# Performance work log

Hardware: AMD Instinct MI355X
Metric: run time of the kernel (lower is better)

## Reference

```python
import jax, jax.numpy as jnp
import numpy as np

NEG_INF = -1e9
START_IDX = 1

def lstm_step(h, c, x_t, Wih, Whh, b):
    g = x_t @ Wih.T + h @ Whh.T + b
    i, f, gg, o = jnp.split(g, 4, axis=-1)  # torch gate order i,f,g,o
    c_new = jax.nn.sigmoid(f) * c + jax.nn.sigmoid(i) * jnp.tanh(gg)
    h_new = jax.nn.sigmoid(o) * jnp.tanh(c_new)
    return h_new, c_new

def masked_lstm(x, valid, Wih, Whh, b):
    # x: [B,S,E], valid: [B,S] bool. Emulates packed-sequence semantics:
    # state frozen and outputs zeroed past each sequence's length.
    B = x.shape[0]; H = Whh.shape[1]
    def step(carry, inp):
        h, c = carry
        x_t, v = inp
        hn, cn = lstm_step(h, c, x_t, Wih, Whh, b)
        v = v[:, None]
        h = jnp.where(v, hn, h); c = jnp.where(v, cn, c)
        return (h, c), jnp.where(v, hn, jnp.zeros_like(hn))
    z = jnp.zeros((B, H), x.dtype)
    (h, c), outs = jax.lax.scan(step, (z, z), (x.transpose(1, 0, 2), valid.T))
    return outs.transpose(1, 0, 2), h, c

def bilstm_encoder(x, lens, Wih_f, Whh_f, b_f, Wih_b, Whh_b, b_b):
    B, S, _ = x.shape
    pos = jnp.arange(S)[None, :]
    valid = pos < lens[:, None]
    out_f, h_f, c_f = masked_lstm(x, valid, Wih_f, Whh_f, b_f)
    # reverse each sequence within its valid length for the backward direction
    rev = jnp.clip(lens[:, None] - 1 - pos, 0, S - 1)  # [B,S]
    x_rev = jnp.take_along_axis(x, rev[:, :, None], axis=1)
    out_r, h_b, c_b = masked_lstm(x_rev, valid, Wih_b, Whh_b, b_b)
    out_b = jnp.take_along_axis(out_r, rev[:, :, None], axis=1) * valid[:, :, None]
    enc = jnp.concatenate([out_f, out_b], -1)          # [B,S,ENC_HID]
    h = jnp.concatenate([h_f, h_b], -1)                # [B,ENC_HID]
    c = jnp.concatenate([c_f, c_b], -1)
    return enc, h, c


def setup_inputs() -> dict:
    key = jax.random.key(0)
    ks = jax.random.split(key, 24)
    B, S, T = 32, 64, 64
    V_SRC, V_TGT, P, E, H2, HD = 50265, 32000, 768, 512, 256, 512
    n = lambda k, sh, s=0.05: (s * jax.random.normal(k, sh)).astype(jnp.float32)
    inp = {
        'xs': jax.random.randint(ks[0], (B, S), 0, V_SRC),
        'x_lens': jax.random.randint(ks[1], (B,), 32, S + 1).astype(jnp.int32),
        'ys': jax.random.randint(ks[2], (B, T + 1), 0, V_TGT),
        'src_emb': n(ks[3], (V_SRC, P)),
        'W_tr': n(ks[4], (E, P)), 'b_tr': jnp.zeros((E,), jnp.float32),
        'Wih_f': n(ks[5], (4 * H2, E)), 'Whh_f': n(ks[6], (4 * H2, H2)), 'b_f': jnp.zeros((4 * H2,), jnp.float32),
        'Wih_b': n(ks[7], (4 * H2, E)), 'Whh_b': n(ks[8], (4 * H2, H2)), 'b_b': jnp.zeros((4 * H2,), jnp.float32),
        'W_attn': n(ks[9], (HD, 2 * HD + HD)), 'b_attn': jnp.zeros((HD,), jnp.float32),
        'v_attn': (jax.random.normal(ks[10], (HD,)) / np.sqrt(HD)).astype(jnp.float32),
        'tgt_emb': n(ks[11], (V_TGT, E)),
        'W_comb': n(ks[12], (HD, E + HD)), 'b_comb': jnp.zeros((HD,), jnp.float32),
        'Wih_d': n(ks[13], (4 * HD, E)), 'Whh_d': n(ks[14], (4 * HD, HD)), 'b_d': jnp.zeros((4 * HD,), jnp.float32),
        'W_out': n(ks[15], (V_TGT, HD)), 'b_out': jnp.zeros((V_TGT,), jnp.float32),
    }
    return inp


def reference(xs, x_lens, ys, src_emb, W_tr, b_tr, Wih_f, Whh_f, b_f,
              Wih_b, Whh_b, b_b, W_attn, b_attn, v_attn, tgt_emb,
              W_comb, b_comb, Wih_d, Whh_d, b_d, W_out, b_out):
    # source embedding (pretrained adapter stub = lookup) + transform
    x = src_emb[xs] @ W_tr.T + b_tr                     # [B,S,E]
    enc, h, c = bilstm_encoder(x, x_lens, Wih_f, Whh_f, b_f, Wih_b, Whh_b, b_b)
    B, S = xs.shape
    T = ys.shape[1] - 1
    HD = Whh_d.shape[1]
    # split attention linear into hidden part and encoder part (precompute latter)
    W_h, W_e = W_attn[:, :2 * HD], W_attn[:, 2 * HD:]
    enc_proj = enc @ W_e.T                              # [B,S,HD]
    src_mask = jnp.arange(S)[None, :] < x_lens[:, None]
    # teacher forcing with ratio 1.0: inputs are [START, ys[:,1:T]]
    tokens = jnp.concatenate([jnp.full((B, 1), START_IDX, ys.dtype), ys[:, 1:T]], axis=1)

    def step(carry, tok):
        h, c = carry
        emb = tgt_emb[tok]                              # [B,E]
        hid = jnp.concatenate([h, c], -1)               # [B,2*HD]
        energy = jnp.tanh(enc_proj + (hid @ W_h.T + b_attn)[:, None, :])
        scores = jnp.where(src_mask, energy @ v_attn, NEG_INF)
        attn = jax.nn.softmax(scores, axis=1)           # [B,S]
        ctx = jnp.einsum('bs,bse->be', attn, enc)
        xi = jax.nn.relu(jnp.concatenate([emb, ctx], -1) @ W_comb.T + b_comb)
        h, c = lstm_step(h, c, xi, Wih_d, Whh_d, b_d)
        out = jax.nn.log_softmax(h @ W_out.T + b_out, axis=-1)
        return (h, c), out

    _, outs = jax.lax.scan(step, (h, c), tokens.T)      # outs: [T,B,V]
    return outs.transpose(1, 0, 2)                      # [B,T,V]
```

## Files before the change

kernel.cpp:

```cpp
#include <hip/hip_runtime.h>
#include <math.h>

#define B_  32
#define S_  64
#define T_  64
#define P_  768
#define E_  512
#define H2_ 256
#define G2_ 1024
#define HD_ 512
#define V_  32000
#define NWG 256

__device__ __forceinline__ float sigf(float x) {
    return 1.0f / (1.0f + __expf(-x));
}
__device__ __forceinline__ float tanh_fast(float x) {
    return 1.0f - 2.0f / (__expf(2.0f * x) + 1.0f);
}

__global__ void k_prep(const int* __restrict__ ys,
                       const float* __restrict__ Whh_f, const float* __restrict__ Whh_b,
                       float* __restrict__ WhhT_f, float* __restrict__ WhhT_b,
                       int* __restrict__ tokens, unsigned* __restrict__ bar)
{
    int i = blockIdx.x * blockDim.x + threadIdx.x;
    int n = gridDim.x * blockDim.x;
    for (int idx = i; idx < G2_ * H2_; idx += n) {
        int k = idx / G2_, g = idx % G2_;
        WhhT_f[idx] = Whh_f[g * H2_ + k];
        WhhT_b[idx] = Whh_b[g * H2_ + k];
    }
    for (int idx = i; idx < T_ * B_; idx += n) {
        int t = idx / B_, b = idx % B_;
        tokens[idx] = (t == 0) ? 1 : ys[b * (T_ + 1) + t];
    }
    for (int idx = i; idx < 160; idx += n) bar[idx] = 0u;
}

__global__ __launch_bounds__(256)
void gemm_f32(const float* __restrict__ A, const int* __restrict__ gidx, int lda,
              const float* __restrict__ W, int ldw, int woff,
              const float* __restrict__ bias,
              float* __restrict__ C, int ldc, int K)
{
    __shared__ __align__(16) float As[16][64];
    __shared__ __align__(16) float Bs[16][64];
    const int m0 = blockIdx.y * 64;
    const int n0 = blockIdx.x * 64;
    const int tid = threadIdx.x;
    const int tm = tid & 15, tn = tid >> 4;
    const int la_m = tid >> 2;
    const int la_k = (tid & 3) * 4;
    float acc[4][4] = {};

    const int am = m0 + la_m;
    const float* arow = A + (long)(gidx ? gidx[am] : am) * lda;
    const float* wrow = W + (long)(n0 + la_m) * ldw + woff;

    for (int k0 = 0; k0 < K; k0 += 16) {
        float4 av = *(const float4*)(arow + k0 + la_k);
        float4 wv = *(const float4*)(wrow + k0 + la_k);
        As[la_k + 0][la_m] = av.x; As[la_k + 1][la_m] = av.y;
        As[la_k + 2][la_m] = av.z; As[la_k + 3][la_m] = av.w;
        Bs[la_k + 0][la_m] = wv.x; Bs[la_k + 1][la_m] = wv.y;
        Bs[la_k + 2][la_m] = wv.z; Bs[la_k + 3][la_m] = wv.w;
        __syncthreads();
        #pragma unroll
        for (int kk = 0; kk < 16; kk++) {
            float4 a = *(const float4*)&As[kk][tm * 4];
            float4 b = *(const float4*)&Bs[kk][tn * 4];
            acc[0][0] += a.x * b.x; acc[0][1] += a.x * b.y; acc[0][2] += a.x * b.z; acc[0][3] += a.x * b.w;
            acc[1][0] += a.y * b.x; acc[1][1] += a.y * b.y; acc[1][2] += a.y * b.z; acc[1][3] += a.y * b.w;
            acc[2][0] += a.z * b.x; acc[2][1] += a.z * b.y; acc[2][2] += a.z * b.z; acc[2][3] += a.z * b.w;
            acc[3][0] += a.w * b.x; acc[3][1] += a.w * b.y; acc[3][2] += a.w * b.z; acc[3][3] += a.w * b.w;
        }
        __syncthreads();
    }
    float b0 = bias ? bias[n0 + tn * 4 + 0] : 0.f;
    float b1 = bias ? bias[n0 + tn * 4 + 1] : 0.f;
    float b2 = bias ? bias[n0 + tn * 4 + 2] : 0.f;
    float b3 = bias ? bias[n0 + tn * 4 + 3] : 0.f;
    #pragma unroll
    for (int i = 0; i < 4; i++) {
        long m = m0 + tm * 4 + i;
        float4 o = make_float4(acc[i][0] + b0, acc[i][1] + b1, acc[i][2] + b2, acc[i][3] + b3);
        *(float4*)&C[m * ldc + n0 + tn * 4] = o;
    }
}

__global__ __launch_bounds__(1024)
void k_encoder(const float* __restrict__ gpre_f, const float* __restrict__ gpre_b,
               const float* __restrict__ WhhT_f, const float* __restrict__ WhhT_b,
               const int* __restrict__ x_lens,
               float* __restrict__ enc, float* __restrict__ hid, float* __restrict__ xh0)
{
    const int b   = blockIdx.x >> 1;
    const int dir = blockIdx.x & 1;
    const float* gpre = dir ? gpre_b : gpre_f;
    const float* WT   = dir ? WhhT_b : WhhT_f;
    const int len = x_lens[b];
    __shared__ float h_lds[H2_];
    __shared__ float g_lds[G2_];
    const int tid = threadIdx.x;
    float c = 0.f;
    if (tid < H2_) h_lds[tid] = 0.f;
    __syncthreads();

    for (int t = 0; t < S_; t++) {
        bool valid = t < len;
        if (valid) {
            int s_in = dir ? (len - 1 - t) : t;
            float acc = gpre[(long)(b * S_ + s_in) * G2_ + tid];
            #pragma unroll 8
            for (int k = 0; k < H2_; k++)
                acc += h_lds[k] * WT[k * G2_ + tid];
            g_lds[tid] = acc;
            __syncthreads();
            if (tid < H2_) {
                float gi = g_lds[tid], gf = g_lds[H2_ + tid];
                float gg = g_lds[2 * H2_ + tid], go = g_lds[3 * H2_ + tid];
                c = sigf(gf) * c + sigf(gi) * tanh_fast(gg);
                float hn = sigf(go) * tanh_fast(c);
                h_lds[tid] = hn;
                enc[(long)(b * S_ + s_in) * E_ + dir * H2_ + tid] = hn;
            }
            __syncthreads();
        } else {
            if (tid < H2_)
                enc[(long)(b * S_ + t) * E_ + dir * H2_ + tid] = 0.f;
        }
    }
    if (tid < H2_) {
        hid[b * 1024 + dir * H2_ + tid]       = h_lds[tid];
        hid[b * 1024 + 512 + dir * H2_ + tid] = c;
        xh0[b * 1024 + 512 + dir * H2_ + tid] = h_lds[tid];
    }
}

__device__ __forceinline__ void grid_bar(unsigned* bar, int w, int tid)
{
    __syncthreads();
    if (tid == 0) {
        __threadfence();
        unsigned a = __hip_atomic_fetch_add(&bar[16 * (w & 7)], 1u,
                        __ATOMIC_RELAXED, __HIP_MEMORY_SCOPE_AGENT);
        unsigned target = (a >> 5) + 1u;
        if ((a & 31u) == 31u) {
            unsigned m = __hip_atomic_fetch_add(&bar[128], 1u,
                            __ATOMIC_RELAXED, __HIP_MEMORY_SCOPE_AGENT);
            if ((m & 7u) == 7u)
                __hip_atomic_store(&bar[144], (m >> 3) + 1u,
                                   __ATOMIC_RELAXED, __HIP_MEMORY_SCOPE_AGENT);
        }
        while (__hip_atomic_load(&bar[144], __ATOMIC_RELAXED,
                                 __HIP_MEMORY_SCOPE_AGENT) < target)
            __builtin_amdgcn_s_sleep(8);
        __threadfence();
    }
    __syncthreads();
}

__global__ __launch_bounds__(256, 1)
void k_decoder(const float* __restrict__ enc, const float* __restrict__ encp,
               const float* __restrict__ embW,
               const float* __restrict__ W_attn, const float* __restrict__ b_attn,
               const float* __restrict__ v_attn, const float* __restrict__ W_comb,
               const float* __restrict__ Wih_d, const float* __restrict__ Whh_d,
               const float* __restrict__ b_d,
               const int* __restrict__ x_lens,
               float* __restrict__ hid, float* __restrict__ xh0,
               float* __restrict__ xh1, float* __restrict__ attq,
               float* __restrict__ ctxg, float* __restrict__ Hall,
               unsigned* __restrict__ bar)
{
    const int w = blockIdx.x;
    const int tid = threadIdx.x;

    __shared__ float WdL[8 * 1028];
    __shared__ float WhL[4 * 1032];
    __shared__ float WcL[4 * 520];
    __shared__ float red[256];
    __shared__ float bsc[832];
    __shared__ float g_l[8 * 33];

    for (int i = tid; i < 8 * 1024; i += 256) {
        int lr = i >> 10, k = i & 1023;
        int row = 512 * (lr & 3) + 2 * w + (lr >> 2);
        WdL[lr * 1028 + k] = (k < 512) ? Wih_d[row * 512 + k]
                                       : Whh_d[row * 512 + (k - 512)];
    }
    for (int i = tid; i < 4 * 1024; i += 256) {
        int lr = i >> 10, k = i & 1023;
        WhL[lr * 1032 + k] = W_attn[(long)(4 * (w >> 1) + lr) * 1536 + k];
    }
    for (int i = tid; i < 4 * 512; i += 256) {
        int lr = i >> 9, k = i & 511;
        WcL[lr * 520 + k] = W_comb[(long)(4 * (w >> 1) + lr) * 1024 + 512 + k];
    }
    __syncthreads();

    const int o  = tid >> 2;
    const int ks = tid & 3;
    const int bl = o >> 2, lr = o & 3;
    const int ab = 16 * (w & 1) + bl;
    const int an = 4 * (w >> 1) + lr;
    const int r8 = tid & 7, b8 = tid >> 3;

    for (int t = 0; t < T_; t++) {
        float* xh_cur  = (t & 1) ? xh1 : xh0;
        float* xh_next = (t & 1) ? xh0 : xh1;

        {
            const float* hr = hid + ab * 1024;
            const float* wr = WhL + lr * 1032;
            float acc = 0.f;
            #pragma unroll 8
            for (int i = 0; i < 64; i++) {
                int k = 16 * i + 4 * ks;
                float4 a = *(const float4*)(hr + k);
                float4 v = *(const float4*)(wr + k);
                acc += a.x * v.x + a.y * v.y + a.z * v.z + a.w * v.w;
            }
            red[tid] = acc;
            __syncthreads();
            if (tid < 64) {
                int b2 = 16 * (w & 1) + (tid >> 2);
                int n2 = 4 * (w >> 1) + (tid & 3);
                float s = red[tid * 4] + red[tid * 4 + 1]
                        + red[tid * 4 + 2] + red[tid * 4 + 3];
                attq[b2 * 512 + n2] = s + b_attn[n2];
            }
        }
        grid_bar(bar, w, tid);

        if (w < 32) {
            float* aq   = bsc;
            float* part = bsc + 512;
            float* p    = bsc + 768;
            aq[tid]       = attq[w * 512 + tid];
            aq[tid + 256] = attq[w * 512 + 256 + tid];
            __syncthreads();
            {
                int s = tid >> 2, q = tid & 3;
                const float* ep = encp + (long)(w * S_ + s) * 512;
                float acc = 0.f;
                #pragma unroll 4
                for (int i = 0; i < 128; i++) {
                    int e = q + 4 * i;
                    acc += v_attn[e] * tanh_fast(ep[e] + aq[e]);
                }
                part[s * 4 + q] = acc;
            }
            __syncthreads();
            if (tid < 64) {
                float sc = part[tid * 4] + part[tid * 4 + 1]
                         + part[tid * 4 + 2] + part[tid * 4 + 3];
                if (tid >= x_lens[w]) sc = -1e9f;
                float m = sc;
                for (int off = 32; off; off >>= 1) m = fmaxf(m, __shfl_xor(m, off));
                float e = __expf(sc - m);
                float sum = e;
                for (int off = 32; off; off >>= 1) sum += __shfl_xor(sum, off);
                p[tid] = e / sum;
            }
            __syncthreads();
            float c0 = 0.f, c1 = 0.f;
            for (int s2 = 0; s2 < S_; s2++) {
                float pp = p[s2];
                const float* er = enc + (long)(w * S_ + s2) * 512;
                c0 += pp * er[tid];
                c1 += pp * er[tid + 256];
            }
            ctxg[w * 512 + tid]       = c0;
            ctxg[w * 512 + 256 + tid] = c1;
        }
        grid_bar(bar, w, tid);

        {
            const float* cr = ctxg + ab * 512;
            const float* wr = WcL + lr * 520;
            float acc = 0.f;
            #pragma unroll 8
            for (int i = 0; i < 32; i++) {
                int k = 16 * i + 4 * ks;
                float4 a = *(const float4*)(cr + k);
                float4 v = *(const float4*)(wr + k);
                acc += a.x * v.x + a.y * v.y + a.z * v.z + a.w * v.w;
            }
            red[tid] = acc;
            __syncthreads();
            if (tid < 64) {
                int b2 = 16 * (w & 1) + (tid >> 2);
                int n2 = 4 * (w >> 1) + (tid & 3);
                float s = red[tid * 4] + red[tid * 4 + 1]
                        + red[tid * 4 + 2] + red[tid * 4 + 3];
                float val = s + embW[((long)t * 32 + b2) * 512 + n2];
                xh_cur[b2 * 1024 + n2] = fmaxf(val, 0.f);
            }
        }
        grid_bar(bar, w, tid);

        {
            const float* ar = xh_cur + b8 * 1024;
            const float* wl = WdL + r8 * 1028;
            float acc = 0.f;
            #pragma unroll 8
            for (int q = 0; q < 256; q++) {
                float4 a = *(const float4*)(ar + 4 * q);
                float4 v = *(const float4*)(wl + 4 * q);
                acc += a.x * v.x + a.y * v.y + a.z * v.z + a.w * v.w;
            }
            int row = 512 * (r8 & 3) + 2 * w + (r8 >> 2);
            g_l[r8 * 33 + b8] = acc + b_d[row];
            __syncthreads();
            if (tid < 64) {
                int bb = tid & 31, hl = tid >> 5;
                int hu = 2 * w + hl;
                float gi = g_l[(hl * 4 + 0) * 33 + bb];
                float gf = g_l[(hl * 4 + 1) * 33 + bb];
                float gg = g_l[(hl * 4 + 2) * 33 + bb];
                float go = g_l[(hl * 4 + 3) * 33 + bb];
                float c_old = hid[bb * 1024 + 512 + hu];
                float c_new = sigf(gf) * c_old + sigf(gi) * tanh_fast(gg);
                float h_new = sigf(go) * tanh_fast(c_new);
                hid[bb * 1024 + hu] = h_new;
                hid[bb * 1024 + 512 + hu] = c_new;
                xh_next[bb * 1024 + 512 + hu] = h_new;
                Hall[((long)bb * T_ + t) * 512 + hu] = h_new;
            }
        }
        grid_bar(bar, w, tid);
    }
}

__global__ __launch_bounds__(256)
void k_lse(const float* __restrict__ Cl, float* __restrict__ lse)
{
    const int r = blockIdx.x;
    const float* row = Cl + (long)r * V_;
    const int tid = threadIdx.x;
    __shared__ float red[4];
    float m = -1e30f;
    for (int i = tid; i < V_; i += 256) m = fmaxf(m, row[i]);
    for (int off = 32; off; off >>= 1) m = fmaxf(m, __shfl_xor(m, off));
    int w = tid >> 6;
    if ((tid & 63) == 0) red[w] = m;
    __syncthreads();
    m = fmaxf(fmaxf(red[0], red[1]), fmaxf(red[2], red[3]));
    __syncthreads();
    float s = 0.f;
    for (int i = tid; i < V_; i += 256) s += __expf(row[i] - m);
    for (int off = 32; off; off >>= 1) s += __shfl_xor(s, off);
    if ((tid & 63) == 0) red[w] = s;
    __syncthreads();
    if (tid == 0) {
        s = red[0] + red[1] + red[2] + red[3];
        lse[r] = m + __logf(s);
    }
}

__global__ void k_logsub(float* __restrict__ C, const float* __restrict__ lse)
{
    long n4 = (long)2048 * V_ / 4;
    long stride = (long)gridDim.x * blockDim.x;
    for (long i = (long)blockIdx.x * blockDim.x + threadIdx.x; i < n4; i += stride) {
        float4 v = ((float4*)C)[i];
        float l = lse[(i * 4) / V_];
        v.x -= l; v.y -= l; v.z -= l; v.w -= l;
        ((float4*)C)[i] = v;
    }
}

extern "C" void kernel_launch(void* const* d_in, const int* in_sizes, int n_in,
                              void* d_out, int out_size, void* d_ws, size_t ws_size,
                              hipStream_t stream)
{
    const int*   xs     = (const int*)  d_in[0];
    const int*   x_lens = (const int*)  d_in[1];
    const int*   ys     = (const int*)  d_in[2];
    const float* src_emb= (const float*)d_in[3];
    const float* W_tr   = (const float*)d_in[4];
    const float* b_tr   = (const float*)d_in[5];
    const float* Wih_f  = (const float*)d_in[6];
    const float* Whh_f  = (const float*)d_in[7];
    const float* b_f    = (const float*)d_in[8];
    const float* Wih_b  = (const float*)d_in[9];
    const float* Whh_b  = (const float*)d_in[10];
    const float* b_b    = (const float*)d_in[11];
    const float* W_attn = (const float*)d_in[12];
    const float* b_attn = (const float*)d_in[13];
    const float* v_attn = (const float*)d_in[14];
    const float* tgt_emb= (const float*)d_in[15];
    const float* W_comb = (const float*)d_in[16];
    const float* b_comb = (const float*)d_in[17];
    const float* Wih_d  = (const float*)d_in[18];
    const float* Whh_d  = (const float*)d_in[19];
    const float* b_d    = (const float*)d_in[20];
    const float* W_out  = (const float*)d_in[21];
    const float* b_out  = (const float*)d_in[22];
    float* out = (float*)d_out;

    float* ws = (float*)d_ws;
    size_t off = 0;
    auto alloc = [&](size_t n) { float* p = ws + off; off += n; return p; };
    float* x      = alloc(2048 * 512);
    float* gpre_f = alloc(2048 * 1024);
    float* gpre_b = alloc(2048 * 1024);
    float* enc    = alloc(2048 * 512);
    float* encp   = alloc(2048 * 512);
    float* embW   = alloc(2048 * 512);
    float* Hall   = alloc(2048 * 512);
    float* hid    = alloc(32 * 1024);
    float* xh0    = alloc(32 * 1024);
    float* xh1    = alloc(32 * 1024);
    float* attq   = alloc(32 * 512);
    float* ctx    = alloc(32 * 512);
    float* WhhTf  = alloc(256 * 1024);
    float* WhhTb  = alloc(256 * 1024);
    float* lse    = alloc(2048);
    int*   tokens = (int*)alloc(2048);
    unsigned* bar = (unsigned*)alloc(160);
    (void)ws_size; (void)n_in; (void)in_sizes; (void)out_size;

    k_prep<<<512, 256, 0, stream>>>(ys, Whh_f, Whh_b, WhhTf, WhhTb, tokens, bar);

    gemm_f32<<<dim3(512 / 64, 2048 / 64), 256, 0, stream>>>(src_emb, xs, P_, W_tr, P_, 0, b_tr, x, 512, P_);
    gemm_f32<<<dim3(1024 / 64, 2048 / 64), 256, 0, stream>>>(x, nullptr, 512, Wih_f, 512, 0, b_f, gpre_f, 1024, 512);
    gemm_f32<<<dim3(1024 / 64, 2048 / 64), 256, 0, stream>>>(x, nullptr, 512, Wih_b, 512, 0, b_b, gpre_b, 1024, 512);

    k_encoder<<<64, 1024, 0, stream>>>(gpre_f, gpre_b, WhhTf, WhhTb, x_lens, enc, hid, xh0);

    gemm_f32<<<dim3(512 / 64, 2048 / 64), 256, 0, stream>>>(enc, nullptr, 512, W_attn, 1536, 1024, nullptr, encp, 512, 512);
    gemm_f32<<<dim3(512 / 64, 2048 / 64), 256, 0, stream>>>(tgt_emb, tokens, 512, W_comb, 1024, 0, b_comb, embW, 512, 512);

    {
        void* args[] = { (void*)&enc, (void*)&encp, (void*)&embW, (void*)&W_attn,
                         (void*)&b_attn, (void*)&v_attn, (void*)&W_comb,
                         (void*)&Wih_d, (void*)&Whh_d, (void*)&b_d, (void*)&x_lens,
                         (void*)&hid, (void*)&xh0, (void*)&xh1, (void*)&attq,
                         (void*)&ctx, (void*)&Hall, (void*)&bar };
        hipLaunchCooperativeKernel((void*)k_decoder, dim3(NWG), dim3(256), args, 0, stream);
    }

    gemm_f32<<<dim3(V_ / 64, 2048 / 64), 256, 0, stream>>>(Hall, nullptr, 512, W_out, 512, 0, b_out, out, V_, 512);
    k_lse<<<2048, 256, 0, stream>>>(out, lse);
    k_logsub<<<8192, 256, 0, stream>>>(out, lse);
}
```

Measured before the change: 8.328 ms.

## Fold context projection into attention blocks, lighten grid barrier, fuse log-softmax

The decoder step now computes the W_comb context projection inside the 32 attention workgroups, which read W_comb from global memory. This drops one grid-wide barrier and the ctx scratch buffer per timestep. The barrier's full threadfences become a vmcnt wait, and shared inter-block data now goes through relaxed agent-scope atomic loads and stores, so cheaper cache behaviour must still keep it coherent. The separate LSE and subtract kernels are merged into one per-row kernel, saving a launch and a pass over the logits.

```diff
diff --git a/kernel.cpp b/kernel.cpp
--- a/kernel.cpp
+++ b/kernel.cpp
@@ -17,6 +17,19 @@
 }
 __device__ __forceinline__ float tanh_fast(float x) {
     return 1.0f - 2.0f / (__expf(2.0f * x) + 1.0f);
+}
+
+__device__ __forceinline__ float ld1(const float* p) {
+    return __hip_atomic_load(p, __ATOMIC_RELAXED, __HIP_MEMORY_SCOPE_AGENT);
+}
+__device__ __forceinline__ float2 ld2(const float* p) {
+    union { unsigned long long u; float2 f; } v;
+    v.u = __hip_atomic_load((const unsigned long long*)p,
+                            __ATOMIC_RELAXED, __HIP_MEMORY_SCOPE_AGENT);
+    return v.f;
+}
+__device__ __forceinline__ void st1(float* p, float v) {
+    __hip_atomic_store(p, v, __ATOMIC_RELAXED, __HIP_MEMORY_SCOPE_AGENT);
 }
 
 __global__ void k_prep(const int* __restrict__ ys,
@@ -142,7 +155,7 @@
 {
     __syncthreads();
     if (tid == 0) {
-        __threadfence();
+        asm volatile("s_waitcnt vmcnt(0)" ::: "memory");
         unsigned a = __hip_atomic_fetch_add(&bar[16 * (w & 7)], 1u,
                         __ATOMIC_RELAXED, __HIP_MEMORY_SCOPE_AGENT);
         unsigned target = (a >> 5) + 1u;
@@ -156,7 +169,7 @@
         while (__hip_atomic_load(&bar[144], __ATOMIC_RELAXED,
                                  __HIP_MEMORY_SCOPE_AGENT) < target)
             __builtin_amdgcn_s_sleep(8);
-        __threadfence();
+        asm volatile("" ::: "memory");
     }
     __syncthreads();
 }
@@ -171,17 +184,15 @@
                const int* __restrict__ x_lens,
                float* __restrict__ hid, float* __restrict__ xh0,
                float* __restrict__ xh1, float* __restrict__ attq,
-               float* __restrict__ ctxg, float* __restrict__ Hall,
-               unsigned* __restrict__ bar)
+               float* __restrict__ Hall, unsigned* __restrict__ bar)
 {
     const int w = blockIdx.x;
     const int tid = threadIdx.x;
 
     __shared__ float WdL[8 * 1028];
     __shared__ float WhL[4 * 1032];
-    __shared__ float WcL[4 * 520];
-    __shared__ float red[256];
-    __shared__ float bsc[832];
+    __shared__ __align__(16) float red[256];
+    __shared__ __align__(16) float bsc[832];
     __shared__ float g_l[8 * 33];
 
     for (int i = tid; i < 8 * 1024; i += 256) {
@@ -194,17 +205,12 @@
         int lr = i >> 10, k = i & 1023;
         WhL[lr * 1032 + k] = W_attn[(long)(4 * (w >> 1) + lr) * 1536 + k];
     }
-    for (int i = tid; i < 4 * 512; i += 256) {
-        int lr = i >> 9, k = i & 511;
-        WcL[lr * 520 + k] = W_comb[(long)(4 * (w >> 1) + lr) * 1024 + 512 + k];
-    }
     __syncthreads();
 
     const int o  = tid >> 2;
     const int ks = tid & 3;
     const int bl = o >> 2, lr = o & 3;
     const int ab = 16 * (w & 1) + bl;
-    const int an = 4 * (w >> 1) + lr;
     const int r8 = tid & 7, b8 = tid >> 3;
 
     for (int t = 0; t < T_; t++) {
@@ -218,9 +224,9 @@
             #pragma unroll 8
             for (int i = 0; i < 64; i++) {
                 int k = 16 * i + 4 * ks;
-                float4 a = *(const float4*)(hr + k);
+                float2 a0 = ld2(hr + k), a1 = ld2(hr + k + 2);
                 float4 v = *(const float4*)(wr + k);
-                acc += a.x * v.x + a.y * v.y + a.z * v.z + a.w * v.w;
+                acc += a0.x * v.x + a0.y * v.y + a1.x * v.z + a1.y * v.w;
             }
             red[tid] = acc;
             __syncthreads();
@@ -229,7 +235,7 @@
                 int n2 = 4 * (w >> 1) + (tid & 3);
                 float s = red[tid * 4] + red[tid * 4 + 1]
                         + red[tid * 4 + 2] + red[tid * 4 + 3];
-                attq[b2 * 512 + n2] = s + b_attn[n2];
+                st1(&attq[b2 * 512 + n2], s + b_attn[n2]);
             }
         }
         grid_bar(bar, w, tid);
@@ -238,8 +244,8 @@
             float* aq   = bsc;
             float* part = bsc + 512;
             float* p    = bsc + 768;
-            aq[tid]       = attq[w * 512 + tid];
-            aq[tid + 256] = attq[w * 512 + 256 + tid];
+            aq[tid]       = ld1(&attq[w * 512 + tid]);
+            aq[tid + 256] = ld1(&attq[w * 512 + 256 + tid]);
             __syncthreads();
             {
                 int s = tid >> 2, q = tid & 3;
@@ -272,32 +278,24 @@
                 c0 += pp * er[tid];
                 c1 += pp * er[tid + 256];
             }
-            ctxg[w * 512 + tid]       = c0;
-            ctxg[w * 512 + 256 + tid] = c1;
-        }
-        grid_bar(bar, w, tid);
-
-        {
-            const float* cr = ctxg + ab * 512;
-            const float* wr = WcL + lr * 520;
-            float acc = 0.f;
-            #pragma unroll 8
-            for (int i = 0; i < 32; i++) {
-                int k = 16 * i + 4 * ks;
-                float4 a = *(const float4*)(cr + k);
-                float4 v = *(const float4*)(wr + k);
-                acc += a.x * v.x + a.y * v.y + a.z * v.z + a.w * v.w;
-            }
-            red[tid] = acc;
-            __syncthreads();
-            if (tid < 64) {
-                int b2 = 16 * (w & 1) + (tid >> 2);
-                int n2 = 4 * (w >> 1) + (tid & 3);
-                float s = red[tid * 4] + red[tid * 4 + 1]
-                        + red[tid * 4 + 2] + red[tid * 4 + 3];
-                float val = s + embW[((long)t * 32 + b2) * 512 + n2];
-                xh_cur[b2 * 1024 + n2] = fmaxf(val, 0.f);
-            }
+            bsc[tid]       = c0;
+            bsc[tid + 256] = c1;
+            __syncthreads();
+            const float* wr0 = W_comb + (long)tid * 1024 + 512;
+            const float* wr1 = W_comb + ((long)tid + 256) * 1024 + 512;
+            float acc0 = 0.f, acc1 = 0.f;
+            #pragma unroll 4
+            for (int k = 0; k < 512; k += 4) {
+                float4 cv  = *(const float4*)&bsc[k];
+                float4 w0v = *(const float4*)(wr0 + k);
+                float4 w1v = *(const float4*)(wr1 + k);
+                acc0 += cv.x * w0v.x + cv.y * w0v.y + cv.z * w0v.z + cv.w * w0v.w;
+                acc1 += cv.x * w1v.x + cv.y * w1v.y + cv.z * w1v.z + cv.w * w1v.w;
+            }
+            float x0 = fmaxf(acc0 + embW[((long)t * 32 + w) * 512 + tid], 0.f);
+            float x1 = fmaxf(acc1 + embW[((long)t * 32 + w) * 512 + 256 + tid], 0.f);
+            st1(&xh_cur[w * 1024 + tid], x0);
+            st1(&xh_cur[w * 1024 + 256 + tid], x1);
         }
         grid_bar(bar, w, tid);
 
@@ -307,9 +305,9 @@
             float acc = 0.f;
             #pragma unroll 8
             for (int q = 0; q < 256; q++) {
-                float4 a = *(const float4*)(ar + 4 * q);
+                float2 a0 = ld2(ar + 4 * q), a1 = ld2(ar + 4 * q + 2);
                 float4 v = *(const float4*)(wl + 4 * q);
-                acc += a.x * v.x + a.y * v.y + a.z * v.z + a.w * v.w;
+                acc += a0.x * v.x + a0.y * v.y + a1.x * v.z + a1.y * v.w;
             }
             int row = 512 * (r8 & 3) + 2 * w + (r8 >> 2);
             g_l[r8 * 33 + b8] = acc + b_d[row];
@@ -321,12 +319,12 @@
                 float gf = g_l[(hl * 4 + 1) * 33 + bb];
                 float gg = g_l[(hl * 4 + 2) * 33 + bb];
                 float go = g_l[(hl * 4 + 3) * 33 + bb];
-                float c_old = hid[bb * 1024 + 512 + hu];
+                float c_old = ld1(&hid[bb * 1024 + 512 + hu]);
                 float c_new = sigf(gf) * c_old + sigf(gi) * tanh_fast(gg);
                 float h_new = sigf(go) * tanh_fast(c_new);
-                hid[bb * 1024 + hu] = h_new;
-                hid[bb * 1024 + 512 + hu] = c_new;
-                xh_next[bb * 1024 + 512 + hu] = h_new;
+                st1(&hid[bb * 1024 + hu], h_new);
+                st1(&hid[bb * 1024 + 512 + hu], c_new);
+                st1(&xh_next[bb * 1024 + 512 + hu], h_new);
                 Hall[((long)bb * T_ + t) * 512 + hu] = h_new;
             }
         }
@@ -335,10 +333,10 @@
 }
 
 __global__ __launch_bounds__(256)
-void k_lse(const float* __restrict__ Cl, float* __restrict__ lse)
+void k_lsesub(float* __restrict__ Cl)
 {
     const int r = blockIdx.x;
-    const float* row = Cl + (long)r * V_;
+    float* row = Cl + (long)r * V_;
     const int tid = threadIdx.x;
     __shared__ float red[4];
     float m = -1e30f;
@@ -354,21 +352,13 @@
     for (int off = 32; off; off >>= 1) s += __shfl_xor(s, off);
     if ((tid & 63) == 0) red[w] = s;
     __syncthreads();
-    if (tid == 0) {
-        s = red[0] + red[1] + red[2] + red[3];
-        lse[r] = m + __logf(s);
-    }
-}
-
-__global__ void k_logsub(float* __restrict__ C, const float* __restrict__ lse)
-{
-    long n4 = (long)2048 * V_ / 4;
-    long stride = (long)gridDim.x * blockDim.x;
-    for (long i = (long)blockIdx.x * blockDim.x + threadIdx.x; i < n4; i += stride) {
-        float4 v = ((float4*)C)[i];
-        float l = lse[(i * 4) / V_];
+    s = red[0] + red[1] + red[2] + red[3];
+    float l = m + __logf(s);
+    float4* r4 = (float4*)row;
+    for (int i = tid; i < V_ / 4; i += 256) {
+        float4 v = r4[i];
         v.x -= l; v.y -= l; v.z -= l; v.w -= l;
-        ((float4*)C)[i] = v;
+        r4[i] = v;
     }
 }
 
@@ -415,10 +405,8 @@
     float* xh0    = alloc(32 * 1024);
     float* xh1    = alloc(32 * 1024);
     float* attq   = alloc(32 * 512);
-    float* ctx    = alloc(32 * 512);
     float* WhhTf  = alloc(256 * 1024);
     float* WhhTb  = alloc(256 * 1024);
-    float* lse    = alloc(2048);
     int*   tokens = (int*)alloc(2048);
     unsigned* bar = (unsigned*)alloc(160);
     (void)ws_size; (void)n_in; (void)in_sizes; (void)out_size;
@@ -439,11 +427,10 @@
                          (void*)&b_attn, (void*)&v_attn, (void*)&W_comb,
                          (void*)&Wih_d, (void*)&Whh_d, (void*)&b_d, (void*)&x_lens,
                          (void*)&hid, (void*)&xh0, (void*)&xh1, (void*)&attq,
-                         (void*)&ctx, (void*)&Hall, (void*)&bar };
+                         (void*)&Hall, (void*)&bar };
         hipLaunchCooperativeKernel((void*)k_decoder, dim3(NWG), dim3(256), args, 0, stream);
     }
 
     gemm_f32<<<dim3(V_ / 64, 2048 / 64), 256, 0, stream>>>(Hall, nullptr, 512, W_out, 512, 0, b_out, out, V_, 512);
-    k_lse<<<2048, 256, 0, stream>>>(out, lse);
-    k_logsub<<<8192, 256, 0, stream>>>(out, lse);
-}
+    k_lsesub<<<2048, 256, 0, stream>>>(out);
+}
```

Measured after the change: 8.290 ms. About the same (-0.5%).
